# Optimization experiments

Hardware: AMD Instinct MI355X
Metric: run time of the kernel (lower is better)

The kernel has to match this reference:

```python
import jax, jax.numpy as jnp
import numpy as np

B, D, H = 65536, 3, 256  # collocation batch, coord dim, hidden width


def setup_inputs() -> dict:
    key = jax.random.key(0)
    ks = jax.random.split(key, 8)

    def init(k, shape, fan_in):
        return jax.random.normal(k, shape, dtype=jnp.float32) * np.float32(1.0 / np.sqrt(fan_in))

    return {
        "x": jax.random.uniform(ks[0], (B, D), dtype=jnp.float32, minval=0.1, maxval=1.0),
        "W0": init(ks[1], (D, H), D), "b0": jnp.zeros((H,), jnp.float32),
        "W1": init(ks[2], (H, H), H), "b1": jnp.zeros((H,), jnp.float32),
        "W2": init(ks[3], (H, H), H), "b2": jnp.zeros((H,), jnp.float32),
        "W3": init(ks[4], (H, H), H), "b3": jnp.zeros((H,), jnp.float32),
        "Wout": init(ks[5], (H, 1), H), "bout": jnp.zeros((1,), jnp.float32),
    }


def reference(x, W0, b0, W1, b1, W2, b2, W3, b3, Wout, bout):
    # Scalar PINN network u(xi), xi: [D]
    def u_fn(xi):
        h = jnp.tanh(xi @ W0 + b0)
        h = jnp.tanh(h @ W1 + b1)
        h = jnp.tanh(h @ W2 + b2)
        h = jnp.tanh(h @ W3 + b3)
        return (h @ Wout + bout)[0]

    u = jax.vmap(u_fn)(x)                               # [B]
    # batch_gradient: du/dx_i for every coordinate axis (Cartesian: no adjustment)
    grads = jax.vmap(jax.grad(u_fn))(x)                 # [B, D]
    # batch_hessian diagonal: d^2u/dx_i^2 via forward-over-reverse
    hess_fn = jax.jacfwd(jax.grad(u_fn))                # [D, D] per sample
    hess_diag = jax.vmap(lambda xi: jnp.diagonal(hess_fn(xi)))(x)  # [B, D]
    # pack (u, grad, hessian-diagonal) as the PDE-residual ingredients
    return jnp.concatenate([u[:, None], grads, hess_diag], axis=1)  # [B, 1+D+D]
```

## Files before the change

### kernel.cpp

```cpp
#include <hip/hip_runtime.h>
#include <hip/hip_fp16.h>

#define HDIM 256
#define MS 16
#define LDAK 264

typedef _Float16 half8 __attribute__((ext_vector_type(8)));
typedef _Float16 half4 __attribute__((ext_vector_type(4)));
typedef float f32x4 __attribute__((ext_vector_type(4)));

__device__ __forceinline__ float fast_tanh(float x) {
    float e = __expf(2.0f * x);
    return 1.0f - 2.0f * __builtin_amdgcn_rcpf(e + 1.0f);
}

__global__ __launch_bounds__(256) void pack_weights(const float* __restrict__ W1,
                                                    const float* __restrict__ W2,
                                                    const float* __restrict__ W3,
                                                    _Float16* __restrict__ out) {
    int tid = blockIdx.x * 256 + threadIdx.x;
    int l = tid >> 13;
    int idx = tid & 8191;
    int kg = idx >> 8;
    int n = idx & 255;
    const float* W = (l == 0) ? W1 : (l == 1) ? W2 : W3;
    half8 v;
    #pragma unroll
    for (int j = 0; j < 8; ++j) v[j] = (_Float16)W[(kg * 8 + j) * 256 + n];
    *(half8*)(out + l * 65536 + (kg * 256 + n) * 8) = v;
}

__global__ __launch_bounds__(256, 2)
void pinn_fused(const float* __restrict__ x,
                const float* __restrict__ W0,
                const float* __restrict__ b0,
                const float* __restrict__ b1,
                const float* __restrict__ b2,
                const float* __restrict__ b3,
                const float* __restrict__ Wout,
                const float* __restrict__ bout,
                const _Float16* __restrict__ Wp,
                float* __restrict__ out) {
    __shared__ __align__(16) _Float16 Abuf[7 * MS][LDAK];
    __shared__ float xs[MS * 3];

    const int tid  = threadIdx.x;
    const int lane = tid & 63;
    const int wid  = tid >> 6;
    const int qd   = lane >> 4;
    const int n15  = lane & 15;
    const int base = blockIdx.x * MS;

    if (tid < MS * 3) xs[tid] = x[base * 3 + tid];
    __syncthreads();

    {
        const int m  = tid & 15;
        const int nb = (tid >> 4) * 16;
        const float x0 = xs[m * 3 + 0], x1 = xs[m * 3 + 1], x2 = xs[m * 3 + 2];
        #pragma unroll
        for (int ch = 0; ch < 2; ++ch) {
            const int n0 = nb + ch * 8;
            half8 h[7];
            #pragma unroll
            for (int r = 0; r < 8; ++r) {
                const int n = n0 + r;
                const float w0 = W0[n], w1 = W0[HDIM + n], w2 = W0[2 * HDIM + n];
                float z  = x0 * w0 + x1 * w1 + x2 * w2 + b0[n];
                float tv = fast_tanh(z);
                float dd = 1.f - tv * tv;
                float c2 = -2.f * tv * dd;
                h[0][r] = (_Float16)tv;
                h[1][r] = (_Float16)(dd * w0);
                h[2][r] = (_Float16)(dd * w1);
                h[3][r] = (_Float16)(dd * w2);
                h[4][r] = (_Float16)(c2 * w0 * w0);
                h[5][r] = (_Float16)(c2 * w1 * w1);
                h[6][r] = (_Float16)(c2 * w2 * w2);
            }
            #pragma unroll
            for (int c = 0; c < 7; ++c)
                *(half8*)&Abuf[c * MS + m][n0] = h[c];
        }
    }
    __syncthreads();

    half8 wf[2][4];
    {
        #pragma unroll
        for (int t = 0; t < 4; ++t) {
            const int n = wid * 64 + t * 16 + n15;
            wf[0][t] = *(const half8*)(Wp + (qd * 256 + n) * 8);
        }
    }

    #pragma unroll
    for (int l = 0; l < 3; ++l) {
        const _Float16* W  = Wp + l * 65536;
        const _Float16* Wn = Wp + (l < 2 ? l + 1 : 2) * 65536;
        const float* bb = (l == 0) ? b1 : (l == 1) ? b2 : b3;

        f32x4 acc[7][4];
        #pragma unroll
        for (int c = 0; c < 7; ++c)
            #pragma unroll
            for (int t = 0; t < 4; ++t) acc[c][t] = (f32x4){0.f, 0.f, 0.f, 0.f};

        half8 af[2][7];
        #pragma unroll
        for (int c = 0; c < 7; ++c)
            af[0][c] = *(const half8*)&Abuf[c * MS + n15][qd * 8];

        #pragma unroll
        for (int s = 0; s < 8; ++s) {
            const int cur = s & 1, nxt = cur ^ 1;
            if (s < 7) {
                #pragma unroll
                for (int t = 0; t < 4; ++t) {
                    const int n = wid * 64 + t * 16 + n15;
                    wf[nxt][t] = *(const half8*)(W + (((s + 1) * 4 + qd) * 256 + n) * 8);
                }
                #pragma unroll
                for (int c = 0; c < 7; ++c)
                    af[nxt][c] = *(const half8*)&Abuf[c * MS + n15][(s + 1) * 32 + qd * 8];
            } else {
                #pragma unroll
                for (int t = 0; t < 4; ++t) {
                    const int n = wid * 64 + t * 16 + n15;
                    wf[nxt][t] = *(const half8*)(Wn + (qd * 256 + n) * 8);
                }
            }
            #pragma unroll
            for (int c = 0; c < 7; ++c)
                #pragma unroll
                for (int t = 0; t < 4; ++t)
                    acc[c][t] = __builtin_amdgcn_mfma_f32_16x16x32_f16(wf[cur][t], af[cur][c], acc[c][t], 0, 0, 0);
        }
        __syncthreads();

        #pragma unroll
        for (int t = 0; t < 4; ++t) {
            const int ncol = wid * 64 + t * 16 + qd * 4;
            f32x4 bv = *(const f32x4*)(bb + ncol);
            half4 h[7];
            #pragma unroll
            for (int r = 0; r < 4; ++r) {
                float zv = acc[0][t][r] + bv[r];
                float tv = fast_tanh(zv);
                float dd = 1.f - tv * tv;
                float c2 = -2.f * tv * dd;
                h[0][r] = (_Float16)tv;
                #pragma unroll
                for (int i = 0; i < 3; ++i) {
                    float zg = acc[1 + i][t][r];
                    float zs = acc[4 + i][t][r];
                    h[1 + i][r] = (_Float16)(dd * zg);
                    h[4 + i][r] = (_Float16)(dd * zs + c2 * zg * zg);
                }
            }
            #pragma unroll
            for (int c = 0; c < 7; ++c)
                *(half4*)&Abuf[c * MS + n15][ncol] = h[c];
        }
        __syncthreads();
    }

    if (tid < 7 * MS * 2) {
        const int row = tid >> 1;
        const int h   = tid & 1;
        const _Float16* rp = &Abuf[row][h * 128];
        const float* wp = Wout + h * 128;
        float accv = 0.f;
        #pragma unroll 4
        for (int k = 0; k < 128; k += 8) {
            half8 av = *(const half8*)&rp[k];
            #pragma unroll
            for (int j = 0; j < 8; ++j) accv += (float)av[j] * wp[k + j];
        }
        accv += __shfl_xor(accv, 1, 64);
        if (h == 0) {
            const int c = row >> 4;
            const int m = row & 15;
            if (c == 0) accv += bout[0];
            out[(base + m) * 7 + c] = accv;
        }
    }
}

extern "C" void kernel_launch(void* const* d_in, const int* in_sizes, int n_in,
                              void* d_out, int out_size, void* d_ws, size_t ws_size,
                              hipStream_t stream) {
    const float* xp   = (const float*)d_in[0];
    const float* W0   = (const float*)d_in[1];
    const float* b0   = (const float*)d_in[2];
    const float* W1   = (const float*)d_in[3];
    const float* b1   = (const float*)d_in[4];
    const float* W2   = (const float*)d_in[5];
    const float* b2   = (const float*)d_in[6];
    const float* W3   = (const float*)d_in[7];
    const float* b3   = (const float*)d_in[8];
    const float* Wout = (const float*)d_in[9];
    const float* bout = (const float*)d_in[10];
    _Float16* Wp = (_Float16*)d_ws;

    pack_weights<<<96, 256, 0, stream>>>(W1, W2, W3, Wp);
    pinn_fused<<<65536 / MS, 256, 0, stream>>>(xp, W0, b0, b1, b2, b3, Wout, bout, Wp,
                                               (float*)d_out);
}
```

Baseline: 262.6 us.

## Triple-buffer weight fragments across layers and hoist first loads above layer-0 prologue

Replaces the double-buffered weight and activation fragment pipeline with a three-deep ring of weight fragments indexed by a global step counter, so weight loads run two K-steps ahead and continue across layer boundaries. The first two weight fragments are loaded before the first-layer prologue to hide global latency behind it. A-fragments are no longer prefetched from LDS but loaded in the same step they are used. The epilogue uses packed round-toward-zero f16 conversion (cvt_pkrtz) instead of per-element casts, which changes rounding slightly and adds register pressure from the third buffer.

```diff
diff --git a/kernel.cpp b/kernel.cpp
--- a/kernel.cpp
+++ b/kernel.cpp
@@ -7,11 +7,19 @@
 
 typedef _Float16 half8 __attribute__((ext_vector_type(8)));
 typedef _Float16 half4 __attribute__((ext_vector_type(4)));
+typedef _Float16 half2v __attribute__((ext_vector_type(2)));
 typedef float f32x4 __attribute__((ext_vector_type(4)));
 
 __device__ __forceinline__ float fast_tanh(float x) {
     float e = __expf(2.0f * x);
     return 1.0f - 2.0f * __builtin_amdgcn_rcpf(e + 1.0f);
+}
+
+__device__ __forceinline__ half4 cvt4(float a, float b, float c, float d) {
+    half2v lo = __builtin_bit_cast(half2v, __builtin_amdgcn_cvt_pkrtz(a, b));
+    half2v hi = __builtin_bit_cast(half2v, __builtin_amdgcn_cvt_pkrtz(c, d));
+    half4 r; r[0] = lo[0]; r[1] = lo[1]; r[2] = hi[0]; r[3] = hi[1];
+    return r;
 }
 
 __global__ __launch_bounds__(256) void pack_weights(const float* __restrict__ W1,
@@ -50,8 +58,18 @@
     const int qd   = lane >> 4;
     const int n15  = lane & 15;
     const int base = blockIdx.x * MS;
+    const int nw   = wid * 64 + n15;
 
     if (tid < MS * 3) xs[tid] = x[base * 3 + tid];
+
+    half8 wf[3][4];
+    #pragma unroll
+    for (int t = 0; t < 4; ++t)
+        wf[0][t] = *(const half8*)(Wp + ((0 * 4 + qd) * 256 + nw + t * 16) * 8);
+    #pragma unroll
+    for (int t = 0; t < 4; ++t)
+        wf[1][t] = *(const half8*)(Wp + ((1 * 4 + qd) * 256 + nw + t * 16) * 8);
+
     __syncthreads();
 
     {
@@ -85,19 +103,8 @@
     }
     __syncthreads();
 
-    half8 wf[2][4];
-    {
-        #pragma unroll
-        for (int t = 0; t < 4; ++t) {
-            const int n = wid * 64 + t * 16 + n15;
-            wf[0][t] = *(const half8*)(Wp + (qd * 256 + n) * 8);
-        }
-    }
-
     #pragma unroll
     for (int l = 0; l < 3; ++l) {
-        const _Float16* W  = Wp + l * 65536;
-        const _Float16* Wn = Wp + (l < 2 ? l + 1 : 2) * 65536;
         const float* bb = (l == 0) ? b1 : (l == 1) ? b2 : b3;
 
         f32x4 acc[7][4];
@@ -106,35 +113,26 @@
             #pragma unroll
             for (int t = 0; t < 4; ++t) acc[c][t] = (f32x4){0.f, 0.f, 0.f, 0.f};
 
-        half8 af[2][7];
-        #pragma unroll
-        for (int c = 0; c < 7; ++c)
-            af[0][c] = *(const half8*)&Abuf[c * MS + n15][qd * 8];
-
         #pragma unroll
         for (int s = 0; s < 8; ++s) {
-            const int cur = s & 1, nxt = cur ^ 1;
-            if (s < 7) {
+            const int g = l * 8 + s;
+            if (g + 2 < 24) {
+                const _Float16* Wn = Wp + ((g + 2) >> 3) * 65536;
+                const int sn = (g + 2) & 7;
                 #pragma unroll
-                for (int t = 0; t < 4; ++t) {
-                    const int n = wid * 64 + t * 16 + n15;
-                    wf[nxt][t] = *(const half8*)(W + (((s + 1) * 4 + qd) * 256 + n) * 8);
-                }
-                #pragma unroll
-                for (int c = 0; c < 7; ++c)
-                    af[nxt][c] = *(const half8*)&Abuf[c * MS + n15][(s + 1) * 32 + qd * 8];
-            } else {
-                #pragma unroll
-                for (int t = 0; t < 4; ++t) {
-                    const int n = wid * 64 + t * 16 + n15;
-                    wf[nxt][t] = *(const half8*)(Wn + (qd * 256 + n) * 8);
-                }
-            }
+                for (int t = 0; t < 4; ++t)
+                    wf[(g + 2) % 3][t] =
+                        *(const half8*)(Wn + ((sn * 4 + qd) * 256 + nw + t * 16) * 8);
+            }
+            half8 af[7];
+            #pragma unroll
+            for (int c = 0; c < 7; ++c)
+                af[c] = *(const half8*)&Abuf[c * MS + n15][s * 32 + qd * 8];
             #pragma unroll
             for (int c = 0; c < 7; ++c)
                 #pragma unroll
                 for (int t = 0; t < 4; ++t)
-                    acc[c][t] = __builtin_amdgcn_mfma_f32_16x16x32_f16(wf[cur][t], af[cur][c], acc[c][t], 0, 0, 0);
+                    acc[c][t] = __builtin_amdgcn_mfma_f32_16x16x32_f16(wf[g % 3][t], af[c], acc[c][t], 0, 0, 0);
         }
         __syncthreads();
 
@@ -142,25 +140,27 @@
         for (int t = 0; t < 4; ++t) {
             const int ncol = wid * 64 + t * 16 + qd * 4;
             f32x4 bv = *(const f32x4*)(bb + ncol);
-            half4 h[7];
+            float tv[4], gj[3][4], sj[3][4];
             #pragma unroll
             for (int r = 0; r < 4; ++r) {
                 float zv = acc[0][t][r] + bv[r];
-                float tv = fast_tanh(zv);
-                float dd = 1.f - tv * tv;
-                float c2 = -2.f * tv * dd;
-                h[0][r] = (_Float16)tv;
+                tv[r] = fast_tanh(zv);
+                float dd = 1.f - tv[r] * tv[r];
+                float c2 = -2.f * tv[r] * dd;
                 #pragma unroll
                 for (int i = 0; i < 3; ++i) {
                     float zg = acc[1 + i][t][r];
                     float zs = acc[4 + i][t][r];
-                    h[1 + i][r] = (_Float16)(dd * zg);
-                    h[4 + i][r] = (_Float16)(dd * zs + c2 * zg * zg);
+                    gj[i][r] = dd * zg;
+                    sj[i][r] = dd * zs + c2 * zg * zg;
                 }
             }
-            #pragma unroll
-            for (int c = 0; c < 7; ++c)
-                *(half4*)&Abuf[c * MS + n15][ncol] = h[c];
+            *(half4*)&Abuf[0 * MS + n15][ncol] = cvt4(tv[0], tv[1], tv[2], tv[3]);
+            #pragma unroll
+            for (int i = 0; i < 3; ++i) {
+                *(half4*)&Abuf[(1 + i) * MS + n15][ncol] = cvt4(gj[i][0], gj[i][1], gj[i][2], gj[i][3]);
+                *(half4*)&Abuf[(4 + i) * MS + n15][ncol] = cvt4(sj[i][0], sj[i][1], sj[i][2], sj[i][3]);
+            }
         }
         __syncthreads();
     }
```

Measured after the change: 255.3 us. 1.03x faster.
